# Kernel optimization log

Measured on AMD Instinct MI355X. Metric: run time of the kernel, lower is better.

## Reference

```python
import jax, jax.numpy as jnp
import numpy as np

NUM_GROUPS = 16
EPS = 1e-05
VARIANCE_FLOOR = 1e-06


def setup_inputs() -> dict:
    key = jax.random.key(0)
    k1, k2, k3, k4 = jax.random.split(key, 4)
    B, L, D, G = 4, 4096, 2048, NUM_GROUPS
    return {
        "x": jax.random.normal(k1, (B, L, D), dtype=jnp.float32),
        "prev_count": jnp.zeros((B,), dtype=jnp.int64 if jax.config.jax_enable_x64 else jnp.int32),
        "prev_mean": jax.random.normal(k2, (B, G), dtype=jnp.float32),
        "prev_var": jnp.ones((B, G), dtype=jnp.float32),
        "padding_mask": jnp.ones((B, L), dtype=bool),
        "weight": 0.1 * jax.random.normal(k3, (D,), dtype=jnp.float32),
        "bias": 0.1 * jax.random.normal(k4, (D,), dtype=jnp.float32),
    }


def reference(x, prev_count, prev_mean, prev_var, padding_mask, weight, bias):
    B, L, D = x.shape
    G = NUM_GROUPS
    gs = D // G
    x_groups = x.reshape(B, L, G, gs)                      # (B,L,G,gs)
    valid = padding_mask.astype(x.dtype)                   # (B,L)
    valid_exp = valid[..., None]                           # (B,L,1)

    group_means = x_groups.mean(axis=-1)                   # (B,L,G)
    prev_count_f = prev_count.astype(x.dtype)              # (B,)
    prev_sum = prev_mean * prev_count_f[:, None]           # (B,G)

    # streaming (cumsum-based Welford) mean
    cumsum_means = jnp.cumsum(group_means * valid_exp, axis=1)
    sum_t = prev_sum[:, None, :] + cumsum_means            # (B,L,G)
    count_t = prev_count_f[:, None] + jnp.cumsum(valid, axis=1)  # (B,L)
    count_clamped = jnp.maximum(count_t, 1.0)
    mean_t = jnp.where(count_t[..., None] > 0.0,
                       sum_t / count_clamped[..., None],
                       prev_mean[:, None, :])               # (B,L,G)

    # Welford M2 accumulation via prefix sums
    mean_prev = jnp.concatenate([prev_mean[:, None, :], mean_t[:, :-1, :]], axis=1)
    delta = group_means - mean_prev
    delta2 = group_means - mean_t
    prev_m2 = prev_var * jnp.maximum(prev_count_f, 1.0)[:, None]  # (B,G)
    m2_t = prev_m2[:, None, :] + jnp.cumsum(delta * delta2 * valid_exp, axis=1)
    var_t = jnp.where(count_t[..., None] > 0.0,
                      m2_t / count_clamped[..., None],
                      prev_var[:, None, :])
    var_t = jnp.maximum(var_t, VARIANCE_FLOOR)

    # normalize + affine
    x_hat = (x_groups - mean_t[..., None]) * jax.lax.rsqrt(var_t[..., None] + EPS)
    scale = (weight + 1.0).reshape(1, 1, G, gs)
    shift = bias.reshape(1, 1, G, gs)
    y = (x_hat * scale + shift).reshape(B, L, D)

    new_count = prev_count + padding_mask.astype(prev_count.dtype).sum(axis=1)
    return y, new_count, mean_t[:, -1, :], var_t[:, -1, :]
```

## Files before the change

### kernel.cpp

```cpp
#include <hip/hip_runtime.h>

#define NGROUPS 16
#define TPG     16
#define CHUNK   32
#define EPS_F   1e-5f
#define VFLOOR  1e-6f

__device__ __forceinline__ float sum8(const float4& a, const float4& b) {
    return ((a.x + a.y) + (a.z + a.w)) + ((b.x + b.y) + (b.z + b.w));
}

__global__ void __launch_bounds__(256)
ts_chunk_agg(const float* __restrict__ x, const int* __restrict__ mask,
             float* __restrict__ loc_n, float* __restrict__ loc_mean,
             float* __restrict__ loc_m2,
             int B, int L, int D, int NC, float inv_gs)
{
    const int b   = blockIdx.x / NC;
    const int c   = blockIdx.x % NC;
    const int tid = threadIdx.x;
    const int g   = tid / TPG;
    const int t0  = c * CHUNK;
    const int t1  = min(t0 + CHUNK, L);

    const float* xb = x + (size_t)b * L * D + tid * 8;
    const int* mb = mask + (size_t)b * L;

    float n = 0.f, mean = 0.f, m2 = 0.f;
    #pragma unroll 4
    for (int t = t0; t < t1; ++t) {
        const float4* p = (const float4*)(xb + (size_t)t * D);
        float4 v0 = p[0], v1 = p[1];
        float s = sum8(v0, v1);
        s += __shfl_xor(s, 1, 64);
        s += __shfl_xor(s, 2, 64);
        s += __shfl_xor(s, 4, 64);
        s += __shfl_xor(s, 8, 64);
        float gm = s * inv_gs;
        if (mb[t]) {
            n += 1.f;
            float d = gm - mean;
            mean += __fdividef(d, n);
            m2 = fmaf(d, gm - mean, m2);
        }
    }
    if ((tid & (TPG - 1)) == 0) {
        int idx = c * (B * NGROUPS) + b * NGROUPS + g;
        loc_n[idx] = n; loc_mean[idx] = mean; loc_m2[idx] = m2;
    }
}

__global__ void ts_scan(const int* __restrict__ prev_count,
                        const float* __restrict__ prev_mean,
                        const float* __restrict__ prev_var,
                        const float* __restrict__ loc_n,
                        const float* __restrict__ loc_mean,
                        const float* __restrict__ loc_m2,
                        float* __restrict__ pref_n, float* __restrict__ pref_mean,
                        float* __restrict__ pref_m2,
                        float* __restrict__ out_count,
                        int B, int NC)
{
    const int chain = threadIdx.x;
    const int BG = B * NGROUPS;
    if (chain >= BG) return;
    const int b = chain / NGROUPS;
    const int g = chain % NGROUPS;

    float n    = (float)prev_count[b];
    float mean = prev_mean[chain];
    float m2   = prev_var[chain] * fmaxf(n, 1.0f);

    for (int c = 0; c < NC; ++c) {
        const int idx = c * BG + chain;
        pref_n[idx] = n; pref_mean[idx] = mean; pref_m2[idx] = m2;
        float nb = loc_n[idx];
        if (nb > 0.f) {
            float mb_ = loc_mean[idx];
            float m2b = loc_m2[idx];
            float nn  = n + nb;
            float d   = mb_ - mean;
            float r   = nb / nn;
            mean += d * r;
            m2   += m2b + d * d * (n * r);
            n = nn;
        }
    }
    if (g == 0) out_count[b] = n;
}

__global__ void __launch_bounds__(256)
ts_norm(const float* __restrict__ x, const int* __restrict__ mask,
        const float* __restrict__ weight, const float* __restrict__ bias,
        const float* __restrict__ pref_n, const float* __restrict__ pref_mean,
        const float* __restrict__ pref_m2,
        float* __restrict__ y, float* __restrict__ out_mean,
        float* __restrict__ out_var,
        int B, int L, int D, int NC, float inv_gs)
{
    const int b   = blockIdx.x / NC;
    const int c   = blockIdx.x % NC;
    const int tid = threadIdx.x;
    const int g   = tid / TPG;
    const int chain = b * NGROUPS + g;
    const int idx   = c * (B * NGROUPS) + chain;

    float n    = pref_n[idx];
    float mean = pref_mean[idx];
    float m2   = pref_m2[idx];

    const float4* wp = (const float4*)(weight + tid * 8);
    const float4* hp = (const float4*)(bias + tid * 8);
    float4 w0 = wp[0], w1 = wp[1];
    float4 h0 = hp[0], h1 = hp[1];
    w0.x += 1.f; w0.y += 1.f; w0.z += 1.f; w0.w += 1.f;
    w1.x += 1.f; w1.y += 1.f; w1.z += 1.f; w1.w += 1.f;

    const int t0 = c * CHUNK;
    const int t1 = min(t0 + CHUNK, L);
    const float* xb = x + (size_t)b * L * D + tid * 8;
    float*       yb = y + (size_t)b * L * D + tid * 8;
    const int* mb = mask + (size_t)b * L;

    float var = VFLOOR;
    #pragma unroll 2
    for (int t = t0; t < t1; ++t) {
        const float4* p = (const float4*)(xb + (size_t)t * D);
        float4 v0 = p[0], v1 = p[1];
        float s = sum8(v0, v1);
        s += __shfl_xor(s, 1, 64);
        s += __shfl_xor(s, 2, 64);
        s += __shfl_xor(s, 4, 64);
        s += __shfl_xor(s, 8, 64);
        float gm = s * inv_gs;
        if (mb[t]) {
            n += 1.f;
            float d = gm - mean;
            mean += __fdividef(d, n);
            m2 = fmaf(d, gm - mean, m2);
        }
        var = fmaxf(__fdividef(m2, fmaxf(n, 1.f)), VFLOOR);
        float rstd = rsqrtf(var + EPS_F);

        float4 o0, o1;
        o0.x = fmaf((v0.x - mean) * rstd, w0.x, h0.x);
        o0.y = fmaf((v0.y - mean) * rstd, w0.y, h0.y);
        o0.z = fmaf((v0.z - mean) * rstd, w0.z, h0.z);
        o0.w = fmaf((v0.w - mean) * rstd, w0.w, h0.w);
        o1.x = fmaf((v1.x - mean) * rstd, w1.x, h1.x);
        o1.y = fmaf((v1.y - mean) * rstd, w1.y, h1.y);
        o1.z = fmaf((v1.z - mean) * rstd, w1.z, h1.z);
        o1.w = fmaf((v1.w - mean) * rstd, w1.w, h1.w);
        float4* q = (float4*)(yb + (size_t)t * D);
        q[0] = o0; q[1] = o1;
    }

    if (c == NC - 1 && (tid & (TPG - 1)) == 0) {
        out_mean[chain] = mean;
        out_var[chain]  = var;
    }
}

extern "C" void kernel_launch(void* const* d_in, const int* in_sizes, int n_in,
                              void* d_out, int out_size, void* d_ws, size_t ws_size,
                              hipStream_t stream) {
    const float* x          = (const float*)d_in[0];
    const int*   prev_count = (const int*)d_in[1];
    const float* prev_mean  = (const float*)d_in[2];
    const float* prev_var   = (const float*)d_in[3];
    const int*   mask       = (const int*)d_in[4];
    const float* weight     = (const float*)d_in[5];
    const float* bias       = (const float*)d_in[6];

    const int B  = in_sizes[1];
    const int D  = in_sizes[5];
    const int L  = in_sizes[4] / B;
    const int NC = (L + CHUNK - 1) / CHUNK;
    const int BG = B * NGROUPS;
    const float inv_gs = (float)NGROUPS / (float)D;

    float* out = (float*)d_out;
    const size_t yN = (size_t)B * L * D;
    float* out_y     = out;
    float* out_count = out + yN;
    float* out_mean  = out + yN + B;
    float* out_var   = out + yN + B + BG;

    float* ws = (float*)d_ws;
    const size_t stride = (size_t)NC * BG;
    float* loc_n     = ws;
    float* loc_mean  = loc_n + stride;
    float* loc_m2    = loc_mean + stride;
    float* pref_n    = loc_m2 + stride;
    float* pref_mean = pref_n + stride;
    float* pref_m2   = pref_mean + stride;

    dim3 blk(D / 8);

    ts_chunk_agg<<<B * NC, blk, 0, stream>>>(x, mask, loc_n, loc_mean, loc_m2,
                                             B, L, D, NC, inv_gs);
    ts_scan<<<1, BG, 0, stream>>>(prev_count, prev_mean, prev_var,
                                  loc_n, loc_mean, loc_m2,
                                  pref_n, pref_mean, pref_m2, out_count, B, NC);
    ts_norm<<<B * NC, blk, 0, stream>>>(x, mask, weight, bias,
                                        pref_n, pref_mean, pref_m2,
                                        out_y, out_mean, out_var,
                                        B, L, D, NC, inv_gs);
}
```

Measured before the change: 331.5 us.

## Split normalization into replay of per-row stats and fully parallel elementwise pass

The first pass now stores per-row group means to a workspace alongside the per-chunk Welford aggregates. A new replay kernel runs one thread per (chunk, group) chain over those stored means to produce per-row mean and rstd, so the sequential Welford walk no longer sits inside the bandwidth-heavy normalize pass. The normalize kernel becomes a grid-stride elementwise loop that only reads x, mean and rstd, which removes the per-row shuffle reductions and the serial dependency inside each block. The scan kernel stages the aggregates in a large dynamic shared-memory buffer and writes the final mean and variance. In exchange there is an extra kernel launch, extra workspace traffic, and a shared-memory request that may exceed launch limits.

```diff
diff --git a/kernel.cpp b/kernel.cpp
--- a/kernel.cpp
+++ b/kernel.cpp
@@ -11,20 +11,21 @@
 }
 
 __global__ void __launch_bounds__(256)
-ts_chunk_agg(const float* __restrict__ x, const int* __restrict__ mask,
-             float* __restrict__ loc_n, float* __restrict__ loc_mean,
-             float* __restrict__ loc_m2,
-             int B, int L, int D, int NC, float inv_gs)
+ts_gm_agg(const float* __restrict__ x, const int* __restrict__ mask,
+          float* __restrict__ gm_buf, float* __restrict__ loc,
+          int B, int L, int D, int NC, float inv_gs)
 {
     const int b   = blockIdx.x / NC;
     const int c   = blockIdx.x % NC;
     const int tid = threadIdx.x;
     const int g   = tid / TPG;
+    const bool leader = (tid & (TPG - 1)) == 0;
     const int t0  = c * CHUNK;
     const int t1  = min(t0 + CHUNK, L);
 
     const float* xb = x + (size_t)b * L * D + tid * 8;
-    const int* mb = mask + (size_t)b * L;
+    const int*   mb = mask + (size_t)b * L;
+    float* gmo = gm_buf + (((size_t)b * NC + c) * NGROUPS + g) * CHUNK;
 
     float n = 0.f, mean = 0.f, m2 = 0.f;
     #pragma unroll 4
@@ -36,33 +37,39 @@
         s += __shfl_xor(s, 2, 64);
         s += __shfl_xor(s, 4, 64);
         s += __shfl_xor(s, 8, 64);
-        float gm = s * inv_gs;
+        float gmv = s * inv_gs;
+        if (leader) gmo[t - t0] = gmv;
         if (mb[t]) {
             n += 1.f;
-            float d = gm - mean;
+            float d = gmv - mean;
             mean += __fdividef(d, n);
-            m2 = fmaf(d, gm - mean, m2);
+            m2 = fmaf(d, gmv - mean, m2);
         }
     }
-    if ((tid & (TPG - 1)) == 0) {
-        int idx = c * (B * NGROUPS) + b * NGROUPS + g;
-        loc_n[idx] = n; loc_mean[idx] = mean; loc_m2[idx] = m2;
+    if (leader) {
+        const int S = NC * B * NGROUPS;
+        const int idx = c * (B * NGROUPS) + b * NGROUPS + g;
+        loc[idx] = n; loc[S + idx] = mean; loc[2 * S + idx] = m2;
     }
 }
 
 __global__ void ts_scan(const int* __restrict__ prev_count,
                         const float* __restrict__ prev_mean,
                         const float* __restrict__ prev_var,
-                        const float* __restrict__ loc_n,
-                        const float* __restrict__ loc_mean,
-                        const float* __restrict__ loc_m2,
-                        float* __restrict__ pref_n, float* __restrict__ pref_mean,
-                        float* __restrict__ pref_m2,
+                        const float* __restrict__ loc,
+                        float* __restrict__ pref,
                         float* __restrict__ out_count,
+                        float* __restrict__ out_mean,
+                        float* __restrict__ out_var,
                         int B, int NC)
 {
+    extern __shared__ float s_loc[];
+    const int BG = B * NGROUPS;
+    const int S  = NC * BG;
+    for (int i = threadIdx.x; i < 3 * S; i += blockDim.x) s_loc[i] = loc[i];
+    __syncthreads();
+
     const int chain = threadIdx.x;
-    const int BG = B * NGROUPS;
     if (chain >= BG) return;
     const int b = chain / NGROUPS;
     const int g = chain % NGROUPS;
@@ -73,11 +80,11 @@
 
     for (int c = 0; c < NC; ++c) {
         const int idx = c * BG + chain;
-        pref_n[idx] = n; pref_mean[idx] = mean; pref_m2[idx] = m2;
-        float nb = loc_n[idx];
+        pref[idx] = n; pref[S + idx] = mean; pref[2 * S + idx] = m2;
+        float nb = s_loc[idx];
         if (nb > 0.f) {
-            float mb_ = loc_mean[idx];
-            float m2b = loc_m2[idx];
+            float mb_ = s_loc[S + idx];
+            float m2b = s_loc[2 * S + idx];
             float nn  = n + nb;
             float d   = mb_ - mean;
             float r   = nb / nn;
@@ -87,61 +94,83 @@
         }
     }
     if (g == 0) out_count[b] = n;
+    out_mean[chain] = mean;
+    out_var[chain]  = fmaxf(__fdividef(m2, fmaxf(n, 1.f)), VFLOOR);
 }
 
 __global__ void __launch_bounds__(256)
-ts_norm(const float* __restrict__ x, const int* __restrict__ mask,
+ts_replay(const int* __restrict__ mask,
+          const float* __restrict__ gm_buf, const float* __restrict__ pref,
+          float* __restrict__ mean_buf, float* __restrict__ rstd_buf,
+          int B, int L, int NC)
+{
+    const int BG  = B * NGROUPS;
+    const int S   = NC * BG;
+    const int tidg = blockIdx.x * blockDim.x + threadIdx.x;
+    if (tidg >= S) return;
+    const int c     = tidg / BG;
+    const int chain = tidg % BG;
+    const int b     = chain / NGROUPS;
+    const int g     = chain % NGROUPS;
+
+    const int idx = c * BG + chain;
+    float n    = pref[idx];
+    float mean = pref[S + idx];
+    float m2   = pref[2 * S + idx];
+
+    const size_t base = (((size_t)b * NC + c) * NGROUPS + g) * CHUNK;
+    const int* mrow = mask + (size_t)b * L + c * CHUNK;
+    const int jmax = min(CHUNK, L - c * CHUNK);
+
+    #pragma unroll 8
+    for (int j = 0; j < jmax; ++j) {
+        float gmv = gm_buf[base + j];
+        if (mrow[j]) {
+            n += 1.f;
+            float d = gmv - mean;
+            mean += __fdividef(d, n);
+            m2 = fmaf(d, gmv - mean, m2);
+        }
+        float var = fmaxf(__fdividef(m2, fmaxf(n, 1.f)), VFLOOR);
+        mean_buf[base + j] = mean;
+        rstd_buf[base + j] = rsqrtf(var + EPS_F);
+    }
+}
+
+__global__ void __launch_bounds__(256)
+ts_norm(const float* __restrict__ x,
         const float* __restrict__ weight, const float* __restrict__ bias,
-        const float* __restrict__ pref_n, const float* __restrict__ pref_mean,
-        const float* __restrict__ pref_m2,
-        float* __restrict__ y, float* __restrict__ out_mean,
-        float* __restrict__ out_var,
-        int B, int L, int D, int NC, float inv_gs)
-{
-    const int b   = blockIdx.x / NC;
-    const int c   = blockIdx.x % NC;
-    const int tid = threadIdx.x;
-    const int g   = tid / TPG;
-    const int chain = b * NGROUPS + g;
-    const int idx   = c * (B * NGROUPS) + chain;
-
-    float n    = pref_n[idx];
-    float mean = pref_mean[idx];
-    float m2   = pref_m2[idx];
-
-    const float4* wp = (const float4*)(weight + tid * 8);
-    const float4* hp = (const float4*)(bias + tid * 8);
+        const float* __restrict__ mean_buf, const float* __restrict__ rstd_buf,
+        float* __restrict__ y,
+        int B, int L, int D, int NC)
+{
+    const int VPR = D / 8;
+    const size_t total = (size_t)B * L * VPR;
+    const size_t stride = (size_t)gridDim.x * blockDim.x;
+    size_t i = (size_t)blockIdx.x * blockDim.x + threadIdx.x;
+    if (i >= total) return;
+
+    const int d8 = (int)(i % VPR);
+    const int g  = d8 / (VPR / NGROUPS);
+
+    const float4* wp = (const float4*)(weight + d8 * 8);
+    const float4* hp = (const float4*)(bias + d8 * 8);
     float4 w0 = wp[0], w1 = wp[1];
     float4 h0 = hp[0], h1 = hp[1];
     w0.x += 1.f; w0.y += 1.f; w0.z += 1.f; w0.w += 1.f;
     w1.x += 1.f; w1.y += 1.f; w1.z += 1.f; w1.w += 1.f;
 
-    const int t0 = c * CHUNK;
-    const int t1 = min(t0 + CHUNK, L);
-    const float* xb = x + (size_t)b * L * D + tid * 8;
-    float*       yb = y + (size_t)b * L * D + tid * 8;
-    const int* mb = mask + (size_t)b * L;
-
-    float var = VFLOOR;
-    #pragma unroll 2
-    for (int t = t0; t < t1; ++t) {
-        const float4* p = (const float4*)(xb + (size_t)t * D);
+    for (; i < total; i += stride) {
+        const size_t row = i / VPR;
+        const int b = (int)(row / L);
+        const int t = (int)(row % L);
+        const int c = t / CHUNK, j = t % CHUNK;
+        const size_t sidx = (((size_t)b * NC + c) * NGROUPS + g) * CHUNK + j;
+        float mean = mean_buf[sidx];
+        float rstd = rstd_buf[sidx];
+
+        const float4* p = (const float4*)(x + i * 8);
         float4 v0 = p[0], v1 = p[1];
-        float s = sum8(v0, v1);
-        s += __shfl_xor(s, 1, 64);
-        s += __shfl_xor(s, 2, 64);
-        s += __shfl_xor(s, 4, 64);
-        s += __shfl_xor(s, 8, 64);
-        float gm = s * inv_gs;
-        if (mb[t]) {
-            n += 1.f;
-            float d = gm - mean;
-            mean += __fdividef(d, n);
-            m2 = fmaf(d, gm - mean, m2);
-        }
-        var = fmaxf(__fdividef(m2, fmaxf(n, 1.f)), VFLOOR);
-        float rstd = rsqrtf(var + EPS_F);
-
         float4 o0, o1;
         o0.x = fmaf((v0.x - mean) * rstd, w0.x, h0.x);
         o0.y = fmaf((v0.y - mean) * rstd, w0.y, h0.y);
@@ -151,13 +180,8 @@
         o1.y = fmaf((v1.y - mean) * rstd, w1.y, h1.y);
         o1.z = fmaf((v1.z - mean) * rstd, w1.z, h1.z);
         o1.w = fmaf((v1.w - mean) * rstd, w1.w, h1.w);
-        float4* q = (float4*)(yb + (size_t)t * D);
+        float4* q = (float4*)(y + i * 8);
         q[0] = o0; q[1] = o1;
-    }
-
-    if (c == NC - 1 && (tid & (TPG - 1)) == 0) {
-        out_mean[chain] = mean;
-        out_var[chain]  = var;
     }
 }
 
@@ -177,6 +201,7 @@
     const int L  = in_sizes[4] / B;
     const int NC = (L + CHUNK - 1) / CHUNK;
     const int BG = B * NGROUPS;
+    const int S  = NC * BG;
     const float inv_gs = (float)NGROUPS / (float)D;
 
     float* out = (float*)d_out;
@@ -187,23 +212,24 @@
     float* out_var   = out + yN + B + BG;
 
     float* ws = (float*)d_ws;
-    const size_t stride = (size_t)NC * BG;
-    float* loc_n     = ws;
-    float* loc_mean  = loc_n + stride;
-    float* loc_m2    = loc_mean + stride;
-    float* pref_n    = loc_m2 + stride;
-    float* pref_mean = pref_n + stride;
-    float* pref_m2   = pref_mean + stride;
+    const size_t gmN = (size_t)B * NC * NGROUPS * CHUNK;
+    float* gm_buf   = ws;
+    float* mean_buf = gm_buf + gmN;
+    float* rstd_buf = mean_buf + gmN;
+    float* loc      = rstd_buf + gmN;
+    float* pref     = loc + 3 * (size_t)S;
 
     dim3 blk(D / 8);
 
-    ts_chunk_agg<<<B * NC, blk, 0, stream>>>(x, mask, loc_n, loc_mean, loc_m2,
-                                             B, L, D, NC, inv_gs);
-    ts_scan<<<1, BG, 0, stream>>>(prev_count, prev_mean, prev_var,
-                                  loc_n, loc_mean, loc_m2,
-                                  pref_n, pref_mean, pref_m2, out_count, B, NC);
-    ts_norm<<<B * NC, blk, 0, stream>>>(x, mask, weight, bias,
-                                        pref_n, pref_mean, pref_m2,
-                                        out_y, out_mean, out_var,
-                                        B, L, D, NC, inv_gs);
-}
+    ts_gm_agg<<<B * NC, blk, 0, stream>>>(x, mask, gm_buf, loc, B, L, D, NC, inv_gs);
+
+    const size_t smem = 3 * (size_t)S * sizeof(float);
+    ts_scan<<<1, 256, smem, stream>>>(prev_count, prev_mean, prev_var, loc, pref,
+                                      out_count, out_mean, out_var, B, NC);
+
+    ts_replay<<<(S + 255) / 256, 256, 0, stream>>>(mask, gm_buf, pref,
+                                                   mean_buf, rstd_buf, B, L, NC);
+
+    ts_norm<<<1024, 256, 0, stream>>>(x, weight, bias, mean_buf, rstd_buf,
+                                      out_y, B, L, D, NC);
+}
```

New measurement: 322.4 us. 2.7% less time.

## Replace serial chunk scan with per-block parallel prefix merge and cached group means

Applied to the files above, without the earlier changes.

Removes the single-block sequential scan kernel. Each normalization block now merges the aggregates of all preceding chunks itself, using a strided lane loop and a shuffle-tree Welford merge. The first kernel also stores per-row group means, so the normalize pass reads them instead of recomputing reductions, and one lane per group precomputes mean/rstd into shared memory. This trades a serial latency-bound launch for redundant O(NC) prefix reads per block and a short serial per-group loop before a barrier.

```diff
diff --git a/kernel.cpp b/kernel.cpp
--- a/kernel.cpp
+++ b/kernel.cpp
@@ -10,21 +10,34 @@
     return ((a.x + a.y) + (a.z + a.w)) + ((b.x + b.y) + (b.z + b.w));
 }
 
+__device__ __forceinline__ void wmerge(float& na, float& ma, float& m2a,
+                                       float nb, float mb, float m2b) {
+    if (nb > 0.f) {
+        float nn = na + nb;
+        float d  = mb - ma;
+        float r  = nb / nn;
+        ma  = fmaf(d, r, ma);
+        m2a = m2a + m2b + d * d * (na * r);
+        na  = nn;
+    }
+}
+
 __global__ void __launch_bounds__(256)
-ts_chunk_agg(const float* __restrict__ x, const int* __restrict__ mask,
-             float* __restrict__ loc_n, float* __restrict__ loc_mean,
-             float* __restrict__ loc_m2,
-             int B, int L, int D, int NC, float inv_gs)
+ts_gm_agg(const float* __restrict__ x, const int* __restrict__ mask,
+          float* __restrict__ gm_buf, float4* __restrict__ loc4,
+          int B, int L, int D, int NC, float inv_gs)
 {
     const int b   = blockIdx.x / NC;
     const int c   = blockIdx.x % NC;
     const int tid = threadIdx.x;
     const int g   = tid / TPG;
+    const bool leader = (tid & (TPG - 1)) == 0;
     const int t0  = c * CHUNK;
     const int t1  = min(t0 + CHUNK, L);
 
     const float* xb = x + (size_t)b * L * D + tid * 8;
-    const int* mb = mask + (size_t)b * L;
+    const int*   mb = mask + (size_t)b * L;
+    float* gmo = gm_buf + (((size_t)b * NC + c) * NGROUPS + g) * CHUNK;
 
     float n = 0.f, mean = 0.f, m2 = 0.f;
     #pragma unroll 4
@@ -36,78 +49,86 @@
         s += __shfl_xor(s, 2, 64);
         s += __shfl_xor(s, 4, 64);
         s += __shfl_xor(s, 8, 64);
-        float gm = s * inv_gs;
+        float gmv = s * inv_gs;
+        if (leader) gmo[t - t0] = gmv;
         if (mb[t]) {
             n += 1.f;
-            float d = gm - mean;
+            float d = gmv - mean;
             mean += __fdividef(d, n);
-            m2 = fmaf(d, gm - mean, m2);
+            m2 = fmaf(d, gmv - mean, m2);
         }
     }
-    if ((tid & (TPG - 1)) == 0) {
-        int idx = c * (B * NGROUPS) + b * NGROUPS + g;
-        loc_n[idx] = n; loc_mean[idx] = mean; loc_m2[idx] = m2;
-    }
-}
-
-__global__ void ts_scan(const int* __restrict__ prev_count,
-                        const float* __restrict__ prev_mean,
-                        const float* __restrict__ prev_var,
-                        const float* __restrict__ loc_n,
-                        const float* __restrict__ loc_mean,
-                        const float* __restrict__ loc_m2,
-                        float* __restrict__ pref_n, float* __restrict__ pref_mean,
-                        float* __restrict__ pref_m2,
-                        float* __restrict__ out_count,
-                        int B, int NC)
+    if (leader) {
+        loc4[((size_t)b * NGROUPS + g) * NC + c] = make_float4(n, mean, m2, 0.f);
+    }
+}
+
+__global__ void __launch_bounds__(256)
+ts_fused(const float* __restrict__ x, const int* __restrict__ mask,
+         const float* __restrict__ gm_buf, const float4* __restrict__ loc4,
+         const int* __restrict__ prev_count, const float* __restrict__ prev_mean,
+         const float* __restrict__ prev_var,
+         const float* __restrict__ weight, const float* __restrict__ bias,
+         float* __restrict__ y, float* __restrict__ out_count,
+         float* __restrict__ out_mean, float* __restrict__ out_var,
+         int B, int L, int D, int NC)
 {
-    const int chain = threadIdx.x;
-    const int BG = B * NGROUPS;
-    if (chain >= BG) return;
-    const int b = chain / NGROUPS;
-    const int g = chain % NGROUPS;
-
-    float n    = (float)prev_count[b];
-    float mean = prev_mean[chain];
-    float m2   = prev_var[chain] * fmaxf(n, 1.0f);
-
-    for (int c = 0; c < NC; ++c) {
-        const int idx = c * BG + chain;
-        pref_n[idx] = n; pref_mean[idx] = mean; pref_m2[idx] = m2;
-        float nb = loc_n[idx];
-        if (nb > 0.f) {
-            float mb_ = loc_mean[idx];
-            float m2b = loc_m2[idx];
-            float nn  = n + nb;
-            float d   = mb_ - mean;
-            float r   = nb / nn;
-            mean += d * r;
-            m2   += m2b + d * d * (n * r);
-            n = nn;
-        }
-    }
-    if (g == 0) out_count[b] = n;
-}
-
-__global__ void __launch_bounds__(256)
-ts_norm(const float* __restrict__ x, const int* __restrict__ mask,
-        const float* __restrict__ weight, const float* __restrict__ bias,
-        const float* __restrict__ pref_n, const float* __restrict__ pref_mean,
-        const float* __restrict__ pref_m2,
-        float* __restrict__ y, float* __restrict__ out_mean,
-        float* __restrict__ out_var,
-        int B, int L, int D, int NC, float inv_gs)
-{
+    __shared__ float s_mean[NGROUPS][CHUNK + 1];
+    __shared__ float s_rstd[NGROUPS][CHUNK + 1];
+
     const int b   = blockIdx.x / NC;
     const int c   = blockIdx.x % NC;
     const int tid = threadIdx.x;
     const int g   = tid / TPG;
+    const int k   = tid & (TPG - 1);
     const int chain = b * NGROUPS + g;
-    const int idx   = c * (B * NGROUPS) + chain;
-
-    float n    = pref_n[idx];
-    float mean = pref_mean[idx];
-    float m2   = pref_m2[idx];
+
+    float n = 0.f, mean = 0.f, m2 = 0.f;
+    const float4* lrow = loc4 + (size_t)chain * NC;
+    for (int cp = k; cp < c; cp += TPG) {
+        float4 v = lrow[cp];
+        wmerge(n, mean, m2, v.x, v.y, v.z);
+    }
+    #pragma unroll
+    for (int o = 1; o < TPG; o <<= 1) {
+        float on = __shfl_xor(n, o, 64);
+        float om = __shfl_xor(mean, o, 64);
+        float o2 = __shfl_xor(m2, o, 64);
+        wmerge(n, mean, m2, on, om, o2);
+    }
+    {
+        float pn = (float)prev_count[b];
+        float pm = prev_mean[chain];
+        float p2 = prev_var[chain] * fmaxf(pn, 1.0f);
+        wmerge(pn, pm, p2, n, mean, m2);
+        n = pn; mean = pm; m2 = p2;
+    }
+
+    const int t0 = c * CHUNK;
+    const int jmax = min(CHUNK, L - t0);
+    if (k == 0) {
+        const float* gmo = gm_buf + (((size_t)b * NC + c) * NGROUPS + g) * CHUNK;
+        const int*   mrow = mask + (size_t)b * L + t0;
+        float var = fmaxf(__fdividef(m2, fmaxf(n, 1.f)), VFLOOR);
+        #pragma unroll 8
+        for (int j = 0; j < jmax; ++j) {
+            float gmv = gmo[j];
+            if (mrow[j]) {
+                n += 1.f;
+                float d = gmv - mean;
+                mean += __fdividef(d, n);
+                m2 = fmaf(d, gmv - mean, m2);
+            }
+            var = fmaxf(__fdividef(m2, fmaxf(n, 1.f)), VFLOOR);
+            s_mean[g][j] = mean;
+            s_rstd[g][j] = rsqrtf(var + EPS_F);
+        }
+        if (c == NC - 1) {
+            out_mean[chain] = mean;
+            out_var[chain]  = var;
+            if (g == 0) out_count[b] = n;
+        }
+    }
 
     const float4* wp = (const float4*)(weight + tid * 8);
     const float4* hp = (const float4*)(bias + tid * 8);
@@ -116,48 +137,27 @@
     w0.x += 1.f; w0.y += 1.f; w0.z += 1.f; w0.w += 1.f;
     w1.x += 1.f; w1.y += 1.f; w1.z += 1.f; w1.w += 1.f;
 
-    const int t0 = c * CHUNK;
-    const int t1 = min(t0 + CHUNK, L);
-    const float* xb = x + (size_t)b * L * D + tid * 8;
-    float*       yb = y + (size_t)b * L * D + tid * 8;
-    const int* mb = mask + (size_t)b * L;
-
-    float var = VFLOOR;
+    __syncthreads();
+
+    const float* xb = x + ((size_t)b * L + t0) * D + tid * 8;
+    float*       yb = y + ((size_t)b * L + t0) * D + tid * 8;
     #pragma unroll 2
-    for (int t = t0; t < t1; ++t) {
-        const float4* p = (const float4*)(xb + (size_t)t * D);
+    for (int j = 0; j < jmax; ++j) {
+        float m_ = s_mean[g][j];
+        float r_ = s_rstd[g][j];
+        const float4* p = (const float4*)(xb + (size_t)j * D);
         float4 v0 = p[0], v1 = p[1];
-        float s = sum8(v0, v1);
-        s += __shfl_xor(s, 1, 64);
-        s += __shfl_xor(s, 2, 64);
-        s += __shfl_xor(s, 4, 64);
-        s += __shfl_xor(s, 8, 64);
-        float gm = s * inv_gs;
-        if (mb[t]) {
-            n += 1.f;
-            float d = gm - mean;
-            mean += __fdividef(d, n);
-            m2 = fmaf(d, gm - mean, m2);
-        }
-        var = fmaxf(__fdividef(m2, fmaxf(n, 1.f)), VFLOOR);
-        float rstd = rsqrtf(var + EPS_F);
-
         float4 o0, o1;
-        o0.x = fmaf((v0.x - mean) * rstd, w0.x, h0.x);
-        o0.y = fmaf((v0.y - mean) * rstd, w0.y, h0.y);
-        o0.z = fmaf((v0.z - mean) * rstd, w0.z, h0.z);
-        o0.w = fmaf((v0.w - mean) * rstd, w0.w, h0.w);
-        o1.x = fmaf((v1.x - mean) * rstd, w1.x, h1.x);
-        o1.y = fmaf((v1.y - mean) * rstd, w1.y, h1.y);
-        o1.z = fmaf((v1.z - mean) * rstd, w1.z, h1.z);
-        o1.w = fmaf((v1.w - mean) * rstd, w1.w, h1.w);
-        float4* q = (float4*)(yb + (size_t)t * D);
+        o0.x = fmaf((v0.x - m_) * r_, w0.x, h0.x);
+        o0.y = fmaf((v0.y - m_) * r_, w0.y, h0.y);
+        o0.z = fmaf((v0.z - m_) * r_, w0.z, h0.z);
+        o0.w = fmaf((v0.w - m_) * r_, w0.w, h0.w);
+        o1.x = fmaf((v1.x - m_) * r_, w1.x, h1.x);
+        o1.y = fmaf((v1.y - m_) * r_, w1.y, h1.y);
+        o1.z = fmaf((v1.z - m_) * r_, w1.z, h1.z);
+        o1.w = fmaf((v1.w - m_) * r_, w1.w, h1.w);
+        float4* q = (float4*)(yb + (size_t)j * D);
         q[0] = o0; q[1] = o1;
-    }
-
-    if (c == NC - 1 && (tid & (TPG - 1)) == 0) {
-        out_mean[chain] = mean;
-        out_var[chain]  = var;
     }
 }
 
@@ -187,23 +187,17 @@
     float* out_var   = out + yN + B + BG;
 
     float* ws = (float*)d_ws;
-    const size_t stride = (size_t)NC * BG;
-    float* loc_n     = ws;
-    float* loc_mean  = loc_n + stride;
-    float* loc_m2    = loc_mean + stride;
-    float* pref_n    = loc_m2 + stride;
-    float* pref_mean = pref_n + stride;
-    float* pref_m2   = pref_mean + stride;
+    const size_t gmN = (size_t)B * NC * NGROUPS * CHUNK;
+    float*  gm_buf = ws;
+    float4* loc4   = (float4*)(ws + gmN);
 
     dim3 blk(D / 8);
 
-    ts_chunk_agg<<<B * NC, blk, 0, stream>>>(x, mask, loc_n, loc_mean, loc_m2,
-                                             B, L, D, NC, inv_gs);
-    ts_scan<<<1, BG, 0, stream>>>(prev_count, prev_mean, prev_var,
-                                  loc_n, loc_mean, loc_m2,
-                                  pref_n, pref_mean, pref_m2, out_count, B, NC);
-    ts_norm<<<B * NC, blk, 0, stream>>>(x, mask, weight, bias,
-                                        pref_n, pref_mean, pref_m2,
-                                        out_y, out_mean, out_var,
-                                        B, L, D, NC, inv_gs);
-}
+    ts_gm_agg<<<B * NC, blk, 0, stream>>>(x, mask, gm_buf, loc4, B, L, D, NC, inv_gs);
+
+    ts_fused<<<B * NC, blk, 0, stream>>>(x, mask, gm_buf, loc4,
+                                         prev_count, prev_mean, prev_var,
+                                         weight, bias,
+                                         out_y, out_count, out_mean, out_var,
+                                         B, L, D, NC);
+}
```

Measured after the change: 273.6 us. 1.21x faster.
